# Kernel optimization log

Measured on AMD Instinct MI355X. Metric: run time of the kernel, lower is better.

The kernel has to match this reference:

```python
import jax, jax.numpy as jnp
import numpy as np

HIDDEN = 1024
H = 16        # num query heads
HKV = 4       # num kv heads
GROUPS = H // HKV
D = HIDDEN // H  # head_dim = 64
SW = (63, 0)  # sliding_window (left, right)
W = SW[0] + SW[1] + 1  # window length per query = 64
MAXPOS = 2048


def _sincos_table(num_pos, dim):
    # faithful to create_sinusoidal_positions (incl. final [:, :, :num_pos] slice)
    inv_freq = 1.0 / 10000 ** (np.arange(0, dim, 2, dtype=np.int32) / dim)
    freqs = np.einsum('i,j->ij', np.arange(num_pos, dtype=np.int32), inv_freq).astype(np.float32)
    emb = np.concatenate((freqs, freqs), axis=-1)
    out = np.concatenate((np.sin(emb)[:, None, :], np.cos(emb)[:, None, :]), axis=-1)
    return jnp.asarray(out[:, :, :num_pos])  # [num_pos, 1, 2*dim]

_SINCOS = _sincos_table(MAXPOS, D)


def _rotate_half(x):
    h = x.shape[-1] // 2
    return jnp.concatenate((-x[..., h:], x[..., :h]), axis=-1)


def setup_inputs() -> dict:
    key = jax.random.key(0)
    k0, k1, k2, k3, k4 = jax.random.split(key, 5)
    B, S = 1, 2048
    std = 0.02
    return {
        'hidden_states': jax.random.normal(k0, (B, S, HIDDEN), dtype=jnp.float32),
        'attention_mask': jnp.ones((B, S, 1, W), dtype=jnp.int32),
        'position_ids': jnp.arange(B * S, dtype=jnp.int32).reshape(B, S) % MAXPOS,
        'q_kernel': jax.random.normal(k1, (HIDDEN, H * D), dtype=jnp.float32) * std,
        'k_kernel': jax.random.normal(k2, (HIDDEN, HKV * D), dtype=jnp.float32) * std,
        'v_kernel': jax.random.normal(k3, (HIDDEN, HKV * D), dtype=jnp.float32) * std,
        'o_kernel': jax.random.normal(k4, (HIDDEN, HIDDEN), dtype=jnp.float32) * std,
    }


def reference(hidden_states, attention_mask, position_ids, q_kernel, k_kernel, v_kernel, o_kernel):
    B, S, _ = hidden_states.shape
    # QKV projections (no bias)
    q = (hidden_states @ q_kernel).reshape(B, S, H, D)
    k = (hidden_states @ k_kernel).reshape(B, S, HKV, D)
    v = (hidden_states @ v_kernel).reshape(B, S, HKV, D)
    # rotary embedding; sincos[pos] -> [B,S,1,2D], broadcasts over head axis
    sc = _SINCOS[position_ids]
    sin, cos = jnp.split(sc, 2, axis=-1)
    k = k * cos + _rotate_half(k) * sin
    q = q * cos + _rotate_half(q) * sin
    # GQA: repeat kv heads to match query heads
    k = jnp.repeat(k, GROUPS, axis=2)  # [B,S,H,D]
    v = jnp.repeat(v, GROUPS, axis=2)
    # sliding-window gather: each query position sees W surrounding keys
    k = jnp.pad(k, ((0, 0), SW, (0, 0), (0, 0)))
    v = jnp.pad(v, ((0, 0), SW, (0, 0), (0, 0)))
    idx = jnp.arange(W, dtype=jnp.int32)[None, :] + jnp.arange(S, dtype=jnp.int32)[:, None]  # [S,W]
    kg = k[:, idx]  # [B,S,W,H,D]
    vg = v[:, idx]
    # attention (q_len=1 per position), scores [B,S,H,W]
    scores = jnp.einsum('bshd,bswhd->bshw', q, kg) / jnp.asarray(np.sqrt(D), scores_dtype := jnp.float32)
    neg = jnp.finfo(jnp.float32).min
    m = attention_mask[:, :, 0, :][:, :, None, :]  # [B,S,1,W] broadcast over H
    bias = jnp.where(m > 0, jnp.float32(0.0), neg)
    weights = jax.nn.softmax(scores + bias, axis=-1)
    attn = jnp.einsum('bshw,bswhd->bshd', weights, vg).reshape(B, S, HIDDEN)
    return attn @ o_kernel
```

## Files before the change

kernel.cpp:

```cpp
#include <hip/hip_runtime.h>
#include <hip/hip_bf16.h>
#include <math.h>

#define S        2048
#define HIDDEN   1024
#define NH       16
#define NKV      4
#define HD       64
#define NQKV     1536
#define VW       2128

typedef _Float16 f16x8 __attribute__((ext_vector_type(8)));
typedef _Float16 f16x4 __attribute__((ext_vector_type(4)));
typedef float    f32x4 __attribute__((ext_vector_type(4)));

__global__ __launch_bounds__(256) void prep_kernel(const float* __restrict__ hs, _Float16* __restrict__ hsf16,
                                                   const float* __restrict__ wq, const float* __restrict__ wk,
                                                   const float* __restrict__ wvv, const float* __restrict__ wo,
                                                   _Float16* __restrict__ wqkvT, _Float16* __restrict__ woT,
                                                   const int* __restrict__ pos_ids, float2* __restrict__ rope_tab,
                                                   _Float16* __restrict__ vTs) {
    int bid = blockIdx.x;
    int tid = threadIdx.x;
    if (bid >= 4864) {
        int d = bid - 4864;
        if (tid < 64) vTs[(size_t)d * VW + tid] = (_Float16)0.0f;
        return;
    }
    if (bid >= 4608) {
        int idx = (bid - 4608) * 256 + tid;
        int s = idx >> 5, f = idx & 31;
        double inv = pow(10000.0, -(double)(2 * f) / 64.0);
        float ang = (float)((double)pos_ids[s] * inv);
        float sn, cs;
        sincosf(ang, &sn, &cs);
        rope_tab[idx] = make_float2(sn, cs);
        return;
    }
    if (bid >= 2560) {
        int i = (bid - 2560) * 256 + tid;
        float4 v = ((const float4*)hs)[i];
        f16x4 o = { (_Float16)v.x, (_Float16)v.y, (_Float16)v.z, (_Float16)v.w };
        *(f16x4*)(hsf16 + 4 * (size_t)i) = o;
        return;
    }
    const float* src; _Float16* dst; int Cn, b;
    if (bid < 1024)      { src = wq;  dst = wqkvT;                       Cn = 1024; b = bid; }
    else if (bid < 1280) { src = wk;  dst = wqkvT + (size_t)1024 * 1024; Cn = 256;  b = bid - 1024; }
    else if (bid < 1536) { src = wvv; dst = wqkvT + (size_t)1280 * 1024; Cn = 256;  b = bid - 1280; }
    else                 { src = wo;  dst = woT;                         Cn = 1024; b = bid - 1536; }
    int xb = Cn >> 5;
    int c0 = (b % xb) * 32;
    int r0 = (b / xb) * 32;
    __shared__ float t[32][33];
    int tx = tid & 31, ty = tid >> 5;
#pragma unroll
    for (int i = ty; i < 32; i += 8)
        t[i][tx] = src[(size_t)(r0 + i) * Cn + c0 + tx];
    __syncthreads();
#pragma unroll
    for (int i = ty; i < 32; i += 8)
        dst[(size_t)(c0 + i) * 1024 + r0 + tx] = (_Float16)t[tx][i];
}

__global__ __launch_bounds__(256) void gemm_qkv(const _Float16* __restrict__ A,
                                                const _Float16* __restrict__ BT,
                                                _Float16* __restrict__ qkv,
                                                _Float16* __restrict__ vTs,
                                                const float2* __restrict__ rope_tab) {
    const int K = HIDDEN;
    const int m0   = blockIdx.y * 128;
    const int n0   = blockIdx.x * 64;
    const int tid  = threadIdx.x;
    const int lane = tid & 63;
    const int wv   = tid >> 6;
    const int lr   = lane & 15;
    const int quad = lane >> 4;
    const int wm   = wv * 32;

    __shared__ __align__(16) _Float16 As[2][128 * 72];
    __shared__ __align__(16) _Float16 Bs[2][64 * 72];

    const int ar8 = tid >> 3, ac8 = tid & 7;

    f32x4 acc[2][4] = {};
    uint4 aR[4], bR[2];

#pragma unroll
    for (int i = 0; i < 4; ++i)
        *(uint4*)&As[0][(ar8 + i * 32) * 72 + ac8 * 8] = *(const uint4*)(A + (size_t)(m0 + ar8 + i * 32) * K + ac8 * 8);
#pragma unroll
    for (int i = 0; i < 2; ++i)
        *(uint4*)&Bs[0][(ar8 + i * 32) * 72 + ac8 * 8] = *(const uint4*)(BT + (size_t)(n0 + ar8 + i * 32) * K + ac8 * 8);
    __syncthreads();

    int p = 0;
    for (int k0 = 64; k0 < K; k0 += 64) {
#pragma unroll
        for (int i = 0; i < 4; ++i)
            aR[i] = *(const uint4*)(A + (size_t)(m0 + ar8 + i * 32) * K + k0 + ac8 * 8);
#pragma unroll
        for (int i = 0; i < 2; ++i)
            bR[i] = *(const uint4*)(BT + (size_t)(n0 + ar8 + i * 32) * K + k0 + ac8 * 8);
#pragma unroll
        for (int ks = 0; ks < 2; ++ks) {
            f16x8 a[2], b[4];
#pragma unroll
            for (int i = 0; i < 2; ++i)
                a[i] = *(const f16x8*)&As[p][(wm + i * 16 + lr) * 72 + (ks * 4 + quad) * 8];
#pragma unroll
            for (int j = 0; j < 4; ++j)
                b[j] = *(const f16x8*)&Bs[p][(j * 16 + lr) * 72 + (ks * 4 + quad) * 8];
#pragma unroll
            for (int i = 0; i < 2; ++i)
#pragma unroll
                for (int j = 0; j < 4; ++j)
                    acc[i][j] = __builtin_amdgcn_mfma_f32_16x16x32_f16(a[i], b[j], acc[i][j], 0, 0, 0);
        }
#pragma unroll
        for (int i = 0; i < 4; ++i)
            *(uint4*)&As[p ^ 1][(ar8 + i * 32) * 72 + ac8 * 8] = aR[i];
#pragma unroll
        for (int i = 0; i < 2; ++i)
            *(uint4*)&Bs[p ^ 1][(ar8 + i * 32) * 72 + ac8 * 8] = bR[i];
        __syncthreads();
        p ^= 1;
    }
#pragma unroll
    for (int ks = 0; ks < 2; ++ks) {
        f16x8 a[2], b[4];
#pragma unroll
        for (int i = 0; i < 2; ++i)
            a[i] = *(const f16x8*)&As[p][(wm + i * 16 + lr) * 72 + (ks * 4 + quad) * 8];
#pragma unroll
        for (int j = 0; j < 4; ++j)
            b[j] = *(const f16x8*)&Bs[p][(j * 16 + lr) * 72 + (ks * 4 + quad) * 8];
#pragma unroll
        for (int i = 0; i < 2; ++i)
#pragma unroll
            for (int j = 0; j < 4; ++j)
                acc[i][j] = __builtin_amdgcn_mfma_f32_16x16x32_f16(a[i], b[j], acc[i][j], 0, 0, 0);
    }

    if (n0 < 1280) {
        const bool isq = (n0 < 1024);
#pragma unroll
        for (int i = 0; i < 2; ++i)
#pragma unroll
            for (int r = 0; r < 4; ++r) {
                int s = m0 + wm + i * 16 + quad * 4 + r;
                const float2* tb = rope_tab + (size_t)s * 32;
#pragma unroll
                for (int j = 0; j < 2; ++j) {
                    float2 sc = tb[j * 16 + lr];
                    float lo = acc[i][j][r], hi = acc[i][j + 2][r];
                    float nlo = lo * sc.y - hi * sc.x;
                    float nhi = hi * sc.y + lo * sc.x;
                    if (isq) { nlo *= 0.125f; nhi *= 0.125f; }
                    qkv[(size_t)s * NQKV + n0 + j * 16 + lr]      = (_Float16)nlo;
                    qkv[(size_t)s * NQKV + n0 + 32 + j * 16 + lr] = (_Float16)nhi;
                }
            }
    } else {
#pragma unroll
        for (int i = 0; i < 2; ++i)
#pragma unroll
            for (int j = 0; j < 4; ++j) {
                int d = n0 - 1280 + j * 16 + lr;
                f16x4 h = { (_Float16)acc[i][j][0], (_Float16)acc[i][j][1],
                            (_Float16)acc[i][j][2], (_Float16)acc[i][j][3] };
                *(f16x4*)(vTs + (size_t)d * VW + 64 + m0 + wm + i * 16 + quad * 4) = h;
            }
    }
}

__global__ __launch_bounds__(256) void gemm_o(const _Float16* __restrict__ A,
                                              const _Float16* __restrict__ BT,
                                              float* __restrict__ C) {
    const int K = HIDDEN, N = HIDDEN;
    const int m0   = blockIdx.y * 128;
    const int n0   = blockIdx.x * 64;
    const int tid  = threadIdx.x;
    const int lane = tid & 63;
    const int wv   = tid >> 6;
    const int lr   = lane & 15;
    const int quad = lane >> 4;
    const int wm   = (wv >> 1) * 64;
    const int wn   = (wv & 1) * 32;

    __shared__ __align__(16) _Float16 As[2][128 * 72];
    __shared__ __align__(16) _Float16 Bs[2][64 * 72];

    const int ar8 = tid >> 3, ac8 = tid & 7;
    f32x4 acc[4][2] = {};
    uint4 aR[4], bR[2];

#pragma unroll
    for (int i = 0; i < 4; ++i)
        *(uint4*)&As[0][(ar8 + i * 32) * 72 + ac8 * 8] = *(const uint4*)(A + (size_t)(m0 + ar8 + i * 32) * K + ac8 * 8);
#pragma unroll
    for (int i = 0; i < 2; ++i)
        *(uint4*)&Bs[0][(ar8 + i * 32) * 72 + ac8 * 8] = *(const uint4*)(BT + (size_t)(n0 + ar8 + i * 32) * K + ac8 * 8);
    __syncthreads();

    int p = 0;
    for (int k0 = 64; k0 < K; k0 += 64) {
#pragma unroll
        for (int i = 0; i < 4; ++i)
            aR[i] = *(const uint4*)(A + (size_t)(m0 + ar8 + i * 32) * K + k0 + ac8 * 8);
#pragma unroll
        for (int i = 0; i < 2; ++i)
            bR[i] = *(const uint4*)(BT + (size_t)(n0 + ar8 + i * 32) * K + k0 + ac8 * 8);
#pragma unroll
        for (int ks = 0; ks < 2; ++ks) {
            f16x8 a[4], b[2];
#pragma unroll
            for (int i = 0; i < 4; ++i)
                a[i] = *(const f16x8*)&As[p][(wm + i * 16 + lr) * 72 + (ks * 4 + quad) * 8];
#pragma unroll
            for (int j = 0; j < 2; ++j)
                b[j] = *(const f16x8*)&Bs[p][(wn + j * 16 + lr) * 72 + (ks * 4 + quad) * 8];
#pragma unroll
            for (int i = 0; i < 4; ++i)
#pragma unroll
                for (int j = 0; j < 2; ++j)
                    acc[i][j] = __builtin_amdgcn_mfma_f32_16x16x32_f16(a[i], b[j], acc[i][j], 0, 0, 0);
        }
#pragma unroll
        for (int i = 0; i < 4; ++i)
            *(uint4*)&As[p ^ 1][(ar8 + i * 32) * 72 + ac8 * 8] = aR[i];
#pragma unroll
        for (int i = 0; i < 2; ++i)
            *(uint4*)&Bs[p ^ 1][(ar8 + i * 32) * 72 + ac8 * 8] = bR[i];
        __syncthreads();
        p ^= 1;
    }
#pragma unroll
    for (int ks = 0; ks < 2; ++ks) {
        f16x8 a[4], b[2];
#pragma unroll
        for (int i = 0; i < 4; ++i)
            a[i] = *(const f16x8*)&As[p][(wm + i * 16 + lr) * 72 + (ks * 4 + quad) * 8];
#pragma unroll
        for (int j = 0; j < 2; ++j)
            b[j] = *(const f16x8*)&Bs[p][(wn + j * 16 + lr) * 72 + (ks * 4 + quad) * 8];
#pragma unroll
        for (int i = 0; i < 4; ++i)
#pragma unroll
            for (int j = 0; j < 2; ++j)
                acc[i][j] = __builtin_amdgcn_mfma_f32_16x16x32_f16(a[i], b[j], acc[i][j], 0, 0, 0);
    }
#pragma unroll
    for (int i = 0; i < 4; ++i)
#pragma unroll
        for (int j = 0; j < 2; ++j)
#pragma unroll
            for (int r = 0; r < 4; ++r)
                C[(size_t)(m0 + wm + i * 16 + quad * 4 + r) * N + n0 + wn + j * 16 + lr] = acc[i][j][r];
}

__global__ __launch_bounds__(256) void attn_mfma(const _Float16* __restrict__ qkv,
                                                 const _Float16* __restrict__ vTs,
                                                 const int* __restrict__ mask,
                                                 _Float16* __restrict__ attn_out) {
    const int s0   = blockIdx.x * 16;
    const int g    = blockIdx.y;
    const int tid  = threadIdx.x;
    const int lane = tid & 63;
    const int wv   = tid >> 6;
    const int h    = g * 4 + wv;
    const int lr   = lane & 15;
    const int quad = lane >> 4;

    __shared__ __align__(16) _Float16 K_lds[80 * 72];
    __shared__ __align__(16) _Float16 Vt_lds[64 * 104];
    __shared__ __align__(16) _Float16 P_lds[4][16 * 104];
    __shared__ int M_lds[1024];

    ((int4*)M_lds)[tid] = ((const int4*)(mask + s0 * 64))[tid];

    for (int c = tid; c < 640; c += 256) {
        int r = c >> 3, cc = c & 7;
        int j = s0 - 64 + r;
        f16x8 val = {};
        if (j >= 0)
            val = *(const f16x8*)(qkv + (size_t)j * NQKV + 1024 + g * 64 + cc * 8);
        *(f16x8*)&K_lds[r * 72 + cc * 8] = val;
    }
    for (int c = tid; c < 64 * 12; c += 256) {
        int d = c / 12, ch = c % 12;
        *(f16x8*)&Vt_lds[d * 104 + ch * 8] =
            *(const f16x8*)(vTs + (size_t)(g * 64 + d) * VW + s0 + ch * 8);
    }

    f16x8 qf[2];
#pragma unroll
    for (int ks = 0; ks < 2; ++ks)
        qf[ks] = *(const f16x8*)(qkv + (size_t)(s0 + lr) * NQKV + h * 64 + ks * 32 + quad * 8);
    __syncthreads();

    f32x4 sc[5];
#pragma unroll
    for (int t = 0; t < 5; ++t) {
        f32x4 a = {};
#pragma unroll
        for (int ks = 0; ks < 2; ++ks) {
            f16x8 kf = *(const f16x8*)&K_lds[(t * 16 + lr) * 72 + ks * 32 + quad * 8];
            a = __builtin_amdgcn_mfma_f32_16x16x32_f16(qf[ks], kf, a, 0, 0, 0);
        }
        sc[t] = a;
    }

#pragma unroll
    for (int t = 0; t < 5; ++t)
#pragma unroll
        for (int r = 0; r < 4; ++r) {
            int qi = quad * 4 + r;
            int w  = t * 16 + lr - 1 - qi;
            bool ok = (w >= 0) && (w < 64) && (M_lds[qi * 64 + (w & 63)] > 0);
            sc[t][r] = ok ? sc[t][r] : -1e30f;
        }

    float pr[5][4];
#pragma unroll
    for (int r = 0; r < 4; ++r) {
        float mx = -1e30f;
#pragma unroll
        for (int t = 0; t < 5; ++t) mx = fmaxf(mx, sc[t][r]);
#pragma unroll
        for (int off = 1; off < 16; off <<= 1) mx = fmaxf(mx, __shfl_xor(mx, off));
        float sum = 0.f;
#pragma unroll
        for (int t = 0; t < 5; ++t) { float e = __expf(sc[t][r] - mx); pr[t][r] = e; sum += e; }
#pragma unroll
        for (int off = 1; off < 16; off <<= 1) sum += __shfl_xor(sum, off);
        float rs = 1.0f / sum;
#pragma unroll
        for (int t = 0; t < 5; ++t) pr[t][r] *= rs;
    }

    _Float16* myP = P_lds[wv];
    {
        f16x4 z = {};
        *(f16x4*)&myP[lr * 104 + 80 + quad * 4] = z;
    }
#pragma unroll
    for (int t = 0; t < 5; ++t)
#pragma unroll
        for (int r = 0; r < 4; ++r)
            myP[(quad * 4 + r) * 104 + t * 16 + lr] = (_Float16)pr[t][r];
    __syncthreads();

    f32x4 oacc[4] = {};
#pragma unroll
    for (int ks = 0; ks < 3; ++ks) {
        f16x8 pf = *(const f16x8*)&myP[lr * 104 + ks * 32 + quad * 8];
#pragma unroll
        for (int t = 0; t < 4; ++t) {
            f16x8 vf = *(const f16x8*)&Vt_lds[(t * 16 + lr) * 104 + ks * 32 + quad * 8];
            oacc[t] = __builtin_amdgcn_mfma_f32_16x16x32_f16(pf, vf, oacc[t], 0, 0, 0);
        }
    }
#pragma unroll
    for (int t = 0; t < 4; ++t)
#pragma unroll
        for (int r = 0; r < 4; ++r)
            attn_out[(size_t)(s0 + quad * 4 + r) * HIDDEN + h * 64 + t * 16 + lr] = (_Float16)oacc[t][r];
}

extern "C" void kernel_launch(void* const* d_in, const int* in_sizes, int n_in,
                              void* d_out, int out_size, void* d_ws, size_t ws_size,
                              hipStream_t stream) {
    const float* hs      = (const float*)d_in[0];
    const int*   mask    = (const int*)  d_in[1];
    const int*   pos_ids = (const int*)  d_in[2];
    const float* wq      = (const float*)d_in[3];
    const float* wk      = (const float*)d_in[4];
    const float* wvv     = (const float*)d_in[5];
    const float* wo      = (const float*)d_in[6];
    float* out = (float*)d_out;

    char* ws = (char*)d_ws;
    _Float16* wqkvT   = (_Float16*)(ws + 0);
    _Float16* woT     = (_Float16*)(ws + (3u << 20));
    _Float16* hsf16   = (_Float16*)(ws + (5u << 20));
    _Float16* qkvf16  = (_Float16*)(ws + (9u << 20));
    _Float16* attnf16 = (_Float16*)(ws + (15u << 20));
    _Float16* vTs     = (_Float16*)(ws + (19u << 20));
    float2*   ropeTab = (float2*)  (ws + (21u << 20));

    prep_kernel<<<5120, 256, 0, stream>>>(hs, hsf16, wq, wk, wvv, wo, wqkvT, woT,
                                          pos_ids, ropeTab, vTs);
    gemm_qkv<<<dim3(NQKV / 64, S / 128), 256, 0, stream>>>(hsf16, wqkvT, qkvf16, vTs, ropeTab);
    attn_mfma<<<dim3(S / 16, NKV), 256, 0, stream>>>(qkvf16, vTs, mask, attnf16);
    gemm_o<<<dim3(HIDDEN / 64, S / 128), 256, 0, stream>>>(attnf16, woT, out);
}
```

Before: 119.0 us.

## Use direct global-to-LDS loads with XOR swizzle in QKV and O GEMMs

Replaces the register-staged, double-buffered LDS tile loads in both projection GEMMs with global_load_lds 16-byte direct loads into a single LDS buffer. Padding is replaced by an XOR swizzle on the column chunk to avoid bank conflicts. This removes the VGPR round trip and halves LDS use, which may raise occupancy. In exchange it drops the software prefetch overlap, adding two barriers per k-step with no double buffering.

```diff
diff --git a/kernel.cpp b/kernel.cpp
--- a/kernel.cpp
+++ b/kernel.cpp
@@ -13,6 +13,11 @@
 typedef _Float16 f16x8 __attribute__((ext_vector_type(8)));
 typedef _Float16 f16x4 __attribute__((ext_vector_type(4)));
 typedef float    f32x4 __attribute__((ext_vector_type(4)));
+
+__device__ __forceinline__ void glds16(const void* g, void* l) {
+    __builtin_amdgcn_global_load_lds((const __attribute__((address_space(1))) void*)g,
+                                     (__attribute__((address_space(3))) void*)l, 16, 0, 0);
+}
 
 __global__ __launch_bounds__(256) void prep_kernel(const float* __restrict__ hs, _Float16* __restrict__ hsf16,
                                                    const float* __restrict__ wq, const float* __restrict__ wk,
@@ -77,69 +82,48 @@
     const int lr   = lane & 15;
     const int quad = lane >> 4;
     const int wm   = wv * 32;
-
-    __shared__ __align__(16) _Float16 As[2][128 * 72];
-    __shared__ __align__(16) _Float16 Bs[2][64 * 72];
-
-    const int ar8 = tid >> 3, ac8 = tid & 7;
+    const int dr   = lane >> 3;
+    const int cc   = lane & 7;
+
+    __shared__ __align__(16) _Float16 As[128 * 64];
+    __shared__ __align__(16) _Float16 Bs[64 * 64];
 
     f32x4 acc[2][4] = {};
-    uint4 aR[4], bR[2];
-
-#pragma unroll
-    for (int i = 0; i < 4; ++i)
-        *(uint4*)&As[0][(ar8 + i * 32) * 72 + ac8 * 8] = *(const uint4*)(A + (size_t)(m0 + ar8 + i * 32) * K + ac8 * 8);
-#pragma unroll
-    for (int i = 0; i < 2; ++i)
-        *(uint4*)&Bs[0][(ar8 + i * 32) * 72 + ac8 * 8] = *(const uint4*)(BT + (size_t)(n0 + ar8 + i * 32) * K + ac8 * 8);
-    __syncthreads();
-
-    int p = 0;
-    for (int k0 = 64; k0 < K; k0 += 64) {
-#pragma unroll
-        for (int i = 0; i < 4; ++i)
-            aR[i] = *(const uint4*)(A + (size_t)(m0 + ar8 + i * 32) * K + k0 + ac8 * 8);
-#pragma unroll
-        for (int i = 0; i < 2; ++i)
-            bR[i] = *(const uint4*)(BT + (size_t)(n0 + ar8 + i * 32) * K + k0 + ac8 * 8);
+
+    for (int k0 = 0; k0 < K; k0 += 64) {
+        __syncthreads();
+#pragma unroll
+        for (int t = 0; t < 4; ++t) {
+            int r = wv * 32 + t * 8 + dr;
+            glds16(A + (size_t)(m0 + r) * K + k0 + (cc ^ (r & 7)) * 8,
+                   As + (wv * 32 + t * 8) * 64);
+        }
+#pragma unroll
+        for (int t = 0; t < 2; ++t) {
+            int r = wv * 16 + t * 8 + dr;
+            glds16(BT + (size_t)(n0 + r) * K + k0 + (cc ^ (r & 7)) * 8,
+                   Bs + (wv * 16 + t * 8) * 64);
+        }
+        __syncthreads();
 #pragma unroll
         for (int ks = 0; ks < 2; ++ks) {
             f16x8 a[2], b[4];
 #pragma unroll
-            for (int i = 0; i < 2; ++i)
-                a[i] = *(const f16x8*)&As[p][(wm + i * 16 + lr) * 72 + (ks * 4 + quad) * 8];
-#pragma unroll
-            for (int j = 0; j < 4; ++j)
-                b[j] = *(const f16x8*)&Bs[p][(j * 16 + lr) * 72 + (ks * 4 + quad) * 8];
+            for (int i = 0; i < 2; ++i) {
+                int row = wm + i * 16 + lr;
+                a[i] = *(const f16x8*)&As[row * 64 + ((ks * 4 + quad) ^ (row & 7)) * 8];
+            }
+#pragma unroll
+            for (int j = 0; j < 4; ++j) {
+                int row = j * 16 + lr;
+                b[j] = *(const f16x8*)&Bs[row * 64 + ((ks * 4 + quad) ^ (row & 7)) * 8];
+            }
 #pragma unroll
             for (int i = 0; i < 2; ++i)
 #pragma unroll
                 for (int j = 0; j < 4; ++j)
                     acc[i][j] = __builtin_amdgcn_mfma_f32_16x16x32_f16(a[i], b[j], acc[i][j], 0, 0, 0);
         }
-#pragma unroll
-        for (int i = 0; i < 4; ++i)
-            *(uint4*)&As[p ^ 1][(ar8 + i * 32) * 72 + ac8 * 8] = aR[i];
-#pragma unroll
-        for (int i = 0; i < 2; ++i)
-            *(uint4*)&Bs[p ^ 1][(ar8 + i * 32) * 72 + ac8 * 8] = bR[i];
-        __syncthreads();
-        p ^= 1;
-    }
-#pragma unroll
-    for (int ks = 0; ks < 2; ++ks) {
-        f16x8 a[2], b[4];
-#pragma unroll
-        for (int i = 0; i < 2; ++i)
-            a[i] = *(const f16x8*)&As[p][(wm + i * 16 + lr) * 72 + (ks * 4 + quad) * 8];
-#pragma unroll
-        for (int j = 0; j < 4; ++j)
-            b[j] = *(const f16x8*)&Bs[p][(j * 16 + lr) * 72 + (ks * 4 + quad) * 8];
-#pragma unroll
-        for (int i = 0; i < 2; ++i)
-#pragma unroll
-            for (int j = 0; j < 4; ++j)
-                acc[i][j] = __builtin_amdgcn_mfma_f32_16x16x32_f16(a[i], b[j], acc[i][j], 0, 0, 0);
     }
 
     if (n0 < 1280) {
@@ -187,68 +171,48 @@
     const int quad = lane >> 4;
     const int wm   = (wv >> 1) * 64;
     const int wn   = (wv & 1) * 32;
-
-    __shared__ __align__(16) _Float16 As[2][128 * 72];
-    __shared__ __align__(16) _Float16 Bs[2][64 * 72];
-
-    const int ar8 = tid >> 3, ac8 = tid & 7;
+    const int dr   = lane >> 3;
+    const int cc   = lane & 7;
+
+    __shared__ __align__(16) _Float16 As[128 * 64];
+    __shared__ __align__(16) _Float16 Bs[64 * 64];
+
     f32x4 acc[4][2] = {};
-    uint4 aR[4], bR[2];
-
-#pragma unroll
-    for (int i = 0; i < 4; ++i)
-        *(uint4*)&As[0][(ar8 + i * 32) * 72 + ac8 * 8] = *(const uint4*)(A + (size_t)(m0 + ar8 + i * 32) * K + ac8 * 8);
-#pragma unroll
-    for (int i = 0; i < 2; ++i)
-        *(uint4*)&Bs[0][(ar8 + i * 32) * 72 + ac8 * 8] = *(const uint4*)(BT + (size_t)(n0 + ar8 + i * 32) * K + ac8 * 8);
-    __syncthreads();
-
-    int p = 0;
-    for (int k0 = 64; k0 < K; k0 += 64) {
-#pragma unroll
-        for (int i = 0; i < 4; ++i)
-            aR[i] = *(const uint4*)(A + (size_t)(m0 + ar8 + i * 32) * K + k0 + ac8 * 8);
-#pragma unroll
-        for (int i = 0; i < 2; ++i)
-            bR[i] = *(const uint4*)(BT + (size_t)(n0 + ar8 + i * 32) * K + k0 + ac8 * 8);
+
+    for (int k0 = 0; k0 < K; k0 += 64) {
+        __syncthreads();
+#pragma unroll
+        for (int t = 0; t < 4; ++t) {
+            int r = wv * 32 + t * 8 + dr;
+            glds16(A + (size_t)(m0 + r) * K + k0 + (cc ^ (r & 7)) * 8,
+                   As + (wv * 32 + t * 8) * 64);
+        }
+#pragma unroll
+        for (int t = 0; t < 2; ++t) {
+            int r = wv * 16 + t * 8 + dr;
+            glds16(BT + (size_t)(n0 + r) * K + k0 + (cc ^ (r & 7)) * 8,
+                   Bs + (wv * 16 + t * 8) * 64);
+        }
+        __syncthreads();
 #pragma unroll
         for (int ks = 0; ks < 2; ++ks) {
             f16x8 a[4], b[2];
 #pragma unroll
-            for (int i = 0; i < 4; ++i)
-                a[i] = *(const f16x8*)&As[p][(wm + i * 16 + lr) * 72 + (ks * 4 + quad) * 8];
-#pragma unroll
-            for (int j = 0; j < 2; ++j)
-                b[j] = *(const f16x8*)&Bs[p][(wn + j * 16 + lr) * 72 + (ks * 4 + quad) * 8];
+            for (int i = 0; i < 4; ++i) {
+                int row = wm + i * 16 + lr;
+                a[i] = *(const f16x8*)&As[row * 64 + ((ks * 4 + quad) ^ (row & 7)) * 8];
+            }
+#pragma unroll
+            for (int j = 0; j < 2; ++j) {
+                int row = wn + j * 16 + lr;
+                b[j] = *(const f16x8*)&Bs[row * 64 + ((ks * 4 + quad) ^ (row & 7)) * 8];
+            }
 #pragma unroll
             for (int i = 0; i < 4; ++i)
 #pragma unroll
                 for (int j = 0; j < 2; ++j)
                     acc[i][j] = __builtin_amdgcn_mfma_f32_16x16x32_f16(a[i], b[j], acc[i][j], 0, 0, 0);
         }
-#pragma unroll
-        for (int i = 0; i < 4; ++i)
-            *(uint4*)&As[p ^ 1][(ar8 + i * 32) * 72 + ac8 * 8] = aR[i];
-#pragma unroll
-        for (int i = 0; i < 2; ++i)
-            *(uint4*)&Bs[p ^ 1][(ar8 + i * 32) * 72 + ac8 * 8] = bR[i];
-        __syncthreads();
-        p ^= 1;
-    }
-#pragma unroll
-    for (int ks = 0; ks < 2; ++ks) {
-        f16x8 a[4], b[2];
-#pragma unroll
-        for (int i = 0; i < 4; ++i)
-            a[i] = *(const f16x8*)&As[p][(wm + i * 16 + lr) * 72 + (ks * 4 + quad) * 8];
-#pragma unroll
-        for (int j = 0; j < 2; ++j)
-            b[j] = *(const f16x8*)&Bs[p][(wn + j * 16 + lr) * 72 + (ks * 4 + quad) * 8];
-#pragma unroll
-        for (int i = 0; i < 4; ++i)
-#pragma unroll
-            for (int j = 0; j < 2; ++j)
-                acc[i][j] = __builtin_amdgcn_mfma_f32_16x16x32_f16(a[i], b[j], acc[i][j], 0, 0, 0);
     }
 #pragma unroll
     for (int i = 0; i < 4; ++i)
@@ -280,12 +244,12 @@
     ((int4*)M_lds)[tid] = ((const int4*)(mask + s0 * 64))[tid];
 
     for (int c = tid; c < 640; c += 256) {
-        int r = c >> 3, cc = c & 7;
+        int r = c >> 3, cl = c & 7;
         int j = s0 - 64 + r;
         f16x8 val = {};
         if (j >= 0)
-            val = *(const f16x8*)(qkv + (size_t)j * NQKV + 1024 + g * 64 + cc * 8);
-        *(f16x8*)&K_lds[r * 72 + cc * 8] = val;
+            val = *(const f16x8*)(qkv + (size_t)j * NQKV + 1024 + g * 64 + cl * 8);
+        *(f16x8*)&K_lds[r * 72 + cl * 8] = val;
     }
     for (int c = tid; c < 64 * 12; c += 256) {
         int d = c / 12, ch = c % 12;
```

Measured after the change: 116.3 us. 2.3% less time.
